# Kernel tuning notes

Measured on AMD Instinct MI355X. Metric: run time of the kernel, lower is better.

Reference implementation:

```python
import jax, jax.numpy as jnp
import numpy as np

B, N, T, F, D = 2, 8, 128, 128, 256
EPS = 1e-5


def setup_inputs() -> dict:
    key = jax.random.key(0)
    ks = jax.random.split(key, 8)
    s = 1.0 / np.sqrt(D)
    s2 = 1.0 / np.sqrt(2 * D)
    return {
        "x": jax.random.normal(ks[0], (B, N, D), dtype=jnp.float32),
        "t_emb": jax.random.normal(ks[1], (T, D), dtype=jnp.float32),
        "f_emb": jax.random.normal(ks[2], (F, D), dtype=jnp.float32),
        "ln_g": jnp.ones((D,), dtype=jnp.float32),
        "ln_b": jnp.zeros((D,), dtype=jnp.float32),
        "W1": jax.random.uniform(ks[3], (D, 2 * D), jnp.float32, -s, s),
        "b1": jax.random.uniform(ks[4], (2 * D,), jnp.float32, -s, s),
        "W2": jax.random.uniform(ks[5], (2 * D, 2), jnp.float32, -s2, s2),
        "b2": jax.random.uniform(ks[6], (2,), jnp.float32, -s2, s2),
    }


def reference(x, t_emb, f_emb, ln_g, ln_b, W1, b1, W2, b2):
    # x: [B,N,D]; pos_emb: [T,F,D]; broadcast-add -> [B,N,T,F,D]
    pos = t_emb[:, None, :] + f_emb[None, :, :]            # [T,F,D]
    h = x[:, :, None, None, :] + pos[None, None]           # [B,N,T,F,D]
    # LayerNorm over last dim
    mu = jnp.mean(h, axis=-1, keepdims=True)
    var = jnp.mean(jnp.square(h - mu), axis=-1, keepdims=True)
    h = (h - mu) * jax.lax.rsqrt(var + EPS) * ln_g + ln_b
    # MLP: D -> 2D -> 2
    h = jax.nn.relu(jnp.einsum("bntfd,de->bntfe", h, W1) + b1)
    out = jnp.einsum("bntfe,eo->bntfo", h, W2) + b2        # [B,N,T,F,2]
    return out
```

## Files before the change

kernel.cpp:

```cpp
#include <hip/hip_runtime.h>
#include <stdint.h>


#define D_ 256
#define E_ 512

typedef __attribute__((ext_vector_type(8))) short short8;
typedef __attribute__((ext_vector_type(4))) short short4v;
typedef __attribute__((ext_vector_type(4))) float f32x4;

typedef __attribute__((address_space(1))) void gvoid;
typedef __attribute__((address_space(3))) void lvoid;
#define GLOAD_LDS16(g, l) \
  __builtin_amdgcn_global_load_lds((gvoid*)(g), (lvoid*)(l), 16, 0, 0)

__device__ inline unsigned short f2bf(float f) {
  unsigned int u = __float_as_uint(f);
  u += 0x7fffu + ((u >> 16) & 1u);
  return (unsigned short)(u >> 16);
}
__device__ inline float bf2f(unsigned short h) {
  return __uint_as_float(((unsigned int)h) << 16);
}

__global__ __launch_bounds__(256) void prep(
    const float* __restrict__ x, const float* __restrict__ t_emb,
    const float* __restrict__ f_emb, const float* __restrict__ ln_g,
    const float* __restrict__ ln_b, const float* __restrict__ W1,
    const float* __restrict__ b1, const float* __restrict__ W2,
    unsigned short* __restrict__ Abuf, unsigned short* __restrict__ Bbuf,
    float* __restrict__ GKW, float* __restrict__ sxt,
    float* __restrict__ sqxt, float* __restrict__ sf,
    float* __restrict__ sqf) {
  const int blk = blockIdx.x;
  const int tid = threadIdx.x;
  if (blk < 544) {
    const int l = tid & 63;
    int arow;
    float v0, v1, v2, v3;
    if (blk < 512) {
      const int r = blk * 4 + (tid >> 6);
      const int bn = r >> 7, t = r & 127;
      const float4 xv = *(const float4*)(x + bn * D_ + 4 * l);
      const float4 tv = *(const float4*)(t_emb + t * D_ + 4 * l);
      v0 = xv.x + tv.x; v1 = xv.y + tv.y;
      v2 = xv.z + tv.z; v3 = xv.w + tv.w;
      arow = r;
    } else {
      const int fi = (blk - 512) * 4 + (tid >> 6);
      const float4 fv = *(const float4*)(f_emb + fi * D_ + 4 * l);
      v0 = fv.x; v1 = fv.y; v2 = fv.z; v3 = fv.w;
      arow = 2048 + fi;
    }
    union { unsigned short u[4]; short4v v; } hi, lo;
    hi.u[0] = f2bf(v0); hi.u[1] = f2bf(v1);
    hi.u[2] = f2bf(v2); hi.u[3] = f2bf(v3);
    lo.u[0] = f2bf(v0 - bf2f(hi.u[0]));
    lo.u[1] = f2bf(v1 - bf2f(hi.u[1]));
    lo.u[2] = f2bf(v2 - bf2f(hi.u[2]));
    lo.u[3] = f2bf(v3 - bf2f(hi.u[3]));
    unsigned short* ab = Abuf + arow * 768 + 4 * l;
    *(short4v*)(ab) = hi.v;
    *(short4v*)(ab + 256) = lo.v;
    *(short4v*)(ab + 512) = hi.v;
    float s = (v0 + v1) + (v2 + v3);
    float q = fmaf(v0, v0, fmaf(v1, v1, fmaf(v2, v2, v3 * v3)));
#pragma unroll
    for (int d = 1; d < 64; d <<= 1) {
      s += __shfl_xor(s, d);
      q += __shfl_xor(q, d);
    }
    if (l == 0) {
      if (blk < 512) { sxt[arow] = s; sqxt[arow] = q; }
      else           { sf[arow - 2048] = s; sqf[arow - 2048] = q; }
    }
  } else if (blk < 546) {
    const int e = (blk - 544) * 256 + tid;
    float G = 0.f, Kv = 0.f;
    for (int k = 0; k < 256; ++k) {
      const float w = W1[k * E_ + e];
      G = fmaf(ln_g[k], w, G);
      Kv = fmaf(ln_b[k], w, Kv);
    }
    float4 o;
    o.x = G; o.y = Kv + b1[e];
    o.z = W2[2 * e]; o.w = W2[2 * e + 1];
    *(float4*)(GKW + 4 * e) = o;
  } else {
    const int gidx = (blk - 546) * 256 + tid;
    const int lane = gidx & 63;
    const int jtl = (gidx >> 6) & 3;
    const int cc = gidx >> 8;
    const int ct = cc % 10;
    const int kt = cc / 10;
    const int col = ct * 64 + jtl * 16 + (lane & 15);
    const int kbase = kt * 32 + ((lane >> 4) & 3) * 8;
    union { unsigned short u[8]; short8 v; } fr;
#pragma unroll
    for (int j = 0; j < 8; ++j) {
      const int kk = kbase + j;
      const int term = kk >> 8;
      const int k = kk & 255;
      float v;
      if (col < 512) v = ln_g[k] * W1[k * E_ + col];
      else           v = f_emb[(col - 512) * D_ + k];
      const unsigned short h = f2bf(v);
      fr.u[j] = (term == 2) ? f2bf(v - bf2f(h)) : h;
    }
    *(short8*)(Bbuf + gidx * 8) = fr.v;
  }
}

__global__ __launch_bounds__(256) void gemm3(
    const unsigned short* __restrict__ Abuf,
    const unsigned short* __restrict__ Bbuf, float* __restrict__ U,
    float* __restrict__ C, float* __restrict__ Vt) {
  __shared__ short8 sB[2][256];
  const int tid = threadIdx.x;
  const int wave = tid >> 6, lane = tid & 63;
  const int quad = (lane >> 4) & 3, n16 = lane & 15;
  const int rt = blockIdx.x / 10, ct = blockIdx.x % 10;
  const int rowb = rt * 128 + wave * 32;

  GLOAD_LDS16((const char*)Bbuf + (size_t)ct * 4096 + tid * 16,
              &sB[0][wave * 64]);

  const unsigned short* a0 = Abuf + (size_t)(rowb + n16) * 768 + quad * 8;
  const unsigned short* a1 = a0 + 16 * 768;
  short8 acur0 = *(const short8*)a0;
  short8 acur1 = *(const short8*)a1;

  f32x4 acc[2][4];
#pragma unroll
  for (int j = 0; j < 4; ++j) {
    acc[0][j] = (f32x4){0.f, 0.f, 0.f, 0.f};
    acc[1][j] = (f32x4){0.f, 0.f, 0.f, 0.f};
  }

  for (int kt = 0; kt < 24; ++kt) {
    __syncthreads();
    short8 anxt0 = acur0, anxt1 = acur1;
    if (kt < 23) {
      GLOAD_LDS16(
          (const char*)Bbuf + (size_t)((kt + 1) * 10 + ct) * 4096 + tid * 16,
          &sB[(kt + 1) & 1][wave * 64]);
      anxt0 = *(const short8*)(a0 + (kt + 1) * 32);
      anxt1 = *(const short8*)(a1 + (kt + 1) * 32);
    }
    const short8* bp = &sB[kt & 1][0];
#pragma unroll
    for (int jtl = 0; jtl < 4; ++jtl) {
      const short8 bf = bp[jtl * 64 + lane];
      acc[0][jtl] =
          __builtin_amdgcn_mfma_f32_16x16x32_bf16(acur0, bf, acc[0][jtl], 0, 0, 0);
      acc[1][jtl] =
          __builtin_amdgcn_mfma_f32_16x16x32_bf16(acur1, bf, acc[1][jtl], 0, 0, 0);
    }
    acur0 = anxt0;
    acur1 = anxt1;
  }

#pragma unroll
  for (int g = 0; g < 2; ++g)
#pragma unroll
    for (int jtl = 0; jtl < 4; ++jtl)
#pragma unroll
      for (int r = 0; r < 4; ++r) {
        const float val = acc[g][jtl][r];
        const int grow = rowb + g * 16 + quad * 4 + r;
        const int col = ct * 64 + jtl * 16 + n16;
        if (rt < 16) {
          if (ct < 8) U[grow * 512 + col] = val;
          else        C[grow * 128 + (col - 512)] = val;
        } else if (ct < 8) {
          Vt[col * 128 + (grow - 2048)] = val;
        }
      }
}

__global__ __launch_bounds__(512) void decode2(
    const float* __restrict__ U, const float* __restrict__ Vt,
    const float* __restrict__ C, const float* __restrict__ GKW,
    const float* __restrict__ sxt, const float* __restrict__ sqxt,
    const float* __restrict__ sf, const float* __restrict__ sqf,
    const float* __restrict__ b2, float* __restrict__ out) {
  __shared__ float part[8][64][17];
  const int tid = threadIdx.x;
  const int w = tid >> 6, lane = tid & 63;
  const int bnt0 = blockIdx.x * 4;

  const float2 sf2 = *(const float2*)(sf + 2 * lane);
  const float2 sqf2 = *(const float2*)(sqf + 2 * lane);
  float Ar[4][2], Br[4][2];
#pragma unroll
  for (int ti = 0; ti < 4; ++ti) {
    const float sx = sxt[bnt0 + ti];
    const float sqx = sqxt[bnt0 + ti];
    const float2 c2 = *(const float2*)(C + (bnt0 + ti) * 128 + 2 * lane);
    {
      const float mu = (sx + sf2.x) * (1.f / 256.f);
      const float var = (sqx + 2.f * c2.x + sqf2.x) * (1.f / 256.f) - mu * mu;
      const float rs = rsqrtf(var + 1e-5f);
      Ar[ti][0] = rs; Br[ti][0] = -rs * mu;
    }
    {
      const float mu = (sx + sf2.y) * (1.f / 256.f);
      const float var = (sqx + 2.f * c2.y + sqf2.y) * (1.f / 256.f) - mu * mu;
      const float rs = rsqrtf(var + 1e-5f);
      Ar[ti][1] = rs; Br[ti][1] = -rs * mu;
    }
  }

  float o[4][2][2] = {};
  const int ebase = __builtin_amdgcn_readfirstlane(w * 64);
#pragma unroll 4
  for (int ei = 0; ei < 64; ++ei) {
    const int e = ebase + ei;
    const float4 gkw = *(const float4*)(GKW + 4 * e);
    const float2 v2 = *(const float2*)(Vt + e * 128 + 2 * lane);
#pragma unroll
    for (int ti = 0; ti < 4; ++ti) {
      const float u = U[(bnt0 + ti) * 512 + e];
      const float s0 = u + v2.x, s1 = u + v2.y;
      float y0 = fmaf(Ar[ti][0], s0, fmaf(Br[ti][0], gkw.x, gkw.y));
      float y1 = fmaf(Ar[ti][1], s1, fmaf(Br[ti][1], gkw.x, gkw.y));
      y0 = fmaxf(y0, 0.f);
      y1 = fmaxf(y1, 0.f);
      o[ti][0][0] = fmaf(y0, gkw.z, o[ti][0][0]);
      o[ti][0][1] = fmaf(y0, gkw.w, o[ti][0][1]);
      o[ti][1][0] = fmaf(y1, gkw.z, o[ti][1][0]);
      o[ti][1][1] = fmaf(y1, gkw.w, o[ti][1][1]);
    }
  }

#pragma unroll
  for (int ti = 0; ti < 4; ++ti)
#pragma unroll
    for (int ff = 0; ff < 2; ++ff) {
      part[w][lane][ti * 4 + ff * 2 + 0] = o[ti][ff][0];
      part[w][lane][ti * 4 + ff * 2 + 1] = o[ti][ff][1];
    }
  __syncthreads();

  const int t = tid >> 7, f = tid & 127;
  const int m = f >> 1, ff = f & 1;
  float r0 = b2[0], r1 = b2[1];
#pragma unroll
  for (int w2 = 0; w2 < 8; ++w2) {
    r0 += part[w2][m][t * 4 + ff * 2 + 0];
    r1 += part[w2][m][t * 4 + ff * 2 + 1];
  }
  float2 res;
  res.x = r0;
  res.y = r1;
  *(float2*)(out + ((bnt0 + t) * 128 + f) * 2) = res;
}

extern "C" void kernel_launch(void* const* d_in, const int* in_sizes, int n_in,
                              void* d_out, int out_size, void* d_ws,
                              size_t ws_size, hipStream_t stream) {
  const float* x = (const float*)d_in[0];
  const float* t_emb = (const float*)d_in[1];
  const float* f_emb = (const float*)d_in[2];
  const float* ln_g = (const float*)d_in[3];
  const float* ln_b = (const float*)d_in[4];
  const float* W1 = (const float*)d_in[5];
  const float* b1 = (const float*)d_in[6];
  const float* W2 = (const float*)d_in[7];
  const float* b2 = (const float*)d_in[8];

  char* ws = (char*)d_ws;
  unsigned short* Abuf = (unsigned short*)(ws + 0);
  unsigned short* Bbuf = (unsigned short*)(ws + 3342336);
  float* U    = (float*)(ws + 4325376);
  float* C    = (float*)(ws + 8519680);
  float* Vt   = (float*)(ws + 9568256);
  float* GKW  = (float*)(ws + 9830400);
  float* sxt  = (float*)(ws + 9838592);
  float* sqxt = (float*)(ws + 9846784);
  float* sfp  = (float*)(ws + 9854976);
  float* sqf  = (float*)(ws + 9855488);

  prep<<<786, 256, 0, stream>>>(x, t_emb, f_emb, ln_g, ln_b, W1, b1, W2, Abuf,
                                Bbuf, GKW, sxt, sqxt, sfp, sqf);
  gemm3<<<170, 256, 0, stream>>>(Abuf, Bbuf, U, C, Vt);
  decode2<<<512, 512, 0, stream>>>(U, Vt, C, GKW, sxt, sqxt, sfp, sqf, b2,
                                   (float*)d_out);
}
```

Before: 127.2 us.

## Use static device buffers, drop LDS staging in gemm, split G/K reduction

Replaces the workspace-pointer intermediates with statically allocated __device__ arrays, so the kernels take fewer arguments and see fixed addresses. The gemm kernel drops the double-buffered LDS staging of B via global_load_lds and its per-iteration barrier. It now reads A and B fragments straight from global memory inside a 4-way unrolled loop. The GKW reduction in prep is split into four independent accumulators to shorten the serial FMA chain. The risk is that direct B loads in gemm lose prefetch overlap and repeat global/L2 traffic across waves.

Measured after the change: 118.9 us. 6.5% less time.

```diff
diff --git a/kernel.cpp b/kernel.cpp
--- a/kernel.cpp
+++ b/kernel.cpp
@@ -9,10 +9,16 @@
 typedef __attribute__((ext_vector_type(4))) short short4v;
 typedef __attribute__((ext_vector_type(4))) float f32x4;
 
-typedef __attribute__((address_space(1))) void gvoid;
-typedef __attribute__((address_space(3))) void lvoid;
-#define GLOAD_LDS16(g, l) \
-  __builtin_amdgcn_global_load_lds((gvoid*)(g), (lvoid*)(l), 16, 0, 0)
+__device__ alignas(16) unsigned short g_Abuf[2176 * 768];
+__device__ alignas(16) unsigned short g_Bbuf[768 * 640];
+__device__ alignas(16) float g_U[2048 * 512];
+__device__ alignas(16) float g_C[2048 * 128];
+__device__ alignas(16) float g_Vt[512 * 128];
+__device__ alignas(16) float g_GKW[512 * 4];
+__device__ alignas(16) float g_sxt[2048];
+__device__ alignas(16) float g_sqxt[2048];
+__device__ alignas(16) float g_sf[128];
+__device__ alignas(16) float g_sqf[128];
 
 __device__ inline unsigned short f2bf(float f) {
   unsigned int u = __float_as_uint(f);
@@ -27,11 +33,7 @@
     const float* __restrict__ x, const float* __restrict__ t_emb,
     const float* __restrict__ f_emb, const float* __restrict__ ln_g,
     const float* __restrict__ ln_b, const float* __restrict__ W1,
-    const float* __restrict__ b1, const float* __restrict__ W2,
-    unsigned short* __restrict__ Abuf, unsigned short* __restrict__ Bbuf,
-    float* __restrict__ GKW, float* __restrict__ sxt,
-    float* __restrict__ sqxt, float* __restrict__ sf,
-    float* __restrict__ sqf) {
+    const float* __restrict__ b1, const float* __restrict__ W2) {
   const int blk = blockIdx.x;
   const int tid = threadIdx.x;
   if (blk < 544) {
@@ -59,7 +61,7 @@
     lo.u[1] = f2bf(v1 - bf2f(hi.u[1]));
     lo.u[2] = f2bf(v2 - bf2f(hi.u[2]));
     lo.u[3] = f2bf(v3 - bf2f(hi.u[3]));
-    unsigned short* ab = Abuf + arow * 768 + 4 * l;
+    unsigned short* ab = g_Abuf + arow * 768 + 4 * l;
     *(short4v*)(ab) = hi.v;
     *(short4v*)(ab + 256) = lo.v;
     *(short4v*)(ab + 512) = hi.v;
@@ -71,21 +73,28 @@
       q += __shfl_xor(q, d);
     }
     if (l == 0) {
-      if (blk < 512) { sxt[arow] = s; sqxt[arow] = q; }
-      else           { sf[arow - 2048] = s; sqf[arow - 2048] = q; }
+      if (blk < 512) { g_sxt[arow] = s; g_sqxt[arow] = q; }
+      else           { g_sf[arow - 2048] = s; g_sqf[arow - 2048] = q; }
     }
   } else if (blk < 546) {
     const int e = (blk - 544) * 256 + tid;
-    float G = 0.f, Kv = 0.f;
-    for (int k = 0; k < 256; ++k) {
-      const float w = W1[k * E_ + e];
-      G = fmaf(ln_g[k], w, G);
-      Kv = fmaf(ln_b[k], w, Kv);
+    float G0 = 0.f, G1 = 0.f, G2 = 0.f, G3 = 0.f;
+    float K0 = 0.f, K1 = 0.f, K2 = 0.f, K3 = 0.f;
+    for (int k = 0; k < 256; k += 4) {
+      const float w0 = W1[(k + 0) * E_ + e];
+      const float w1 = W1[(k + 1) * E_ + e];
+      const float w2 = W1[(k + 2) * E_ + e];
+      const float w3 = W1[(k + 3) * E_ + e];
+      G0 = fmaf(ln_g[k + 0], w0, G0); K0 = fmaf(ln_b[k + 0], w0, K0);
+      G1 = fmaf(ln_g[k + 1], w1, G1); K1 = fmaf(ln_b[k + 1], w1, K1);
+      G2 = fmaf(ln_g[k + 2], w2, G2); K2 = fmaf(ln_b[k + 2], w2, K2);
+      G3 = fmaf(ln_g[k + 3], w3, G3); K3 = fmaf(ln_b[k + 3], w3, K3);
     }
     float4 o;
-    o.x = G; o.y = Kv + b1[e];
+    o.x = (G0 + G1) + (G2 + G3);
+    o.y = (K0 + K1) + (K2 + K3) + b1[e];
     o.z = W2[2 * e]; o.w = W2[2 * e + 1];
-    *(float4*)(GKW + 4 * e) = o;
+    *(float4*)(g_GKW + 4 * e) = o;
   } else {
     const int gidx = (blk - 546) * 256 + tid;
     const int lane = gidx & 63;
@@ -107,28 +116,19 @@
       const unsigned short h = f2bf(v);
       fr.u[j] = (term == 2) ? f2bf(v - bf2f(h)) : h;
     }
-    *(short8*)(Bbuf + gidx * 8) = fr.v;
-  }
-}
-
-__global__ __launch_bounds__(256) void gemm3(
-    const unsigned short* __restrict__ Abuf,
-    const unsigned short* __restrict__ Bbuf, float* __restrict__ U,
-    float* __restrict__ C, float* __restrict__ Vt) {
-  __shared__ short8 sB[2][256];
+    *(short8*)(g_Bbuf + gidx * 8) = fr.v;
+  }
+}
+
+__global__ __launch_bounds__(256) void gemm3() {
   const int tid = threadIdx.x;
   const int wave = tid >> 6, lane = tid & 63;
   const int quad = (lane >> 4) & 3, n16 = lane & 15;
   const int rt = blockIdx.x / 10, ct = blockIdx.x % 10;
   const int rowb = rt * 128 + wave * 32;
 
-  GLOAD_LDS16((const char*)Bbuf + (size_t)ct * 4096 + tid * 16,
-              &sB[0][wave * 64]);
-
-  const unsigned short* a0 = Abuf + (size_t)(rowb + n16) * 768 + quad * 8;
+  const unsigned short* a0 = g_Abuf + (size_t)(rowb + n16) * 768 + quad * 8;
   const unsigned short* a1 = a0 + 16 * 768;
-  short8 acur0 = *(const short8*)a0;
-  short8 acur1 = *(const short8*)a1;
 
   f32x4 acc[2][4];
 #pragma unroll
@@ -137,27 +137,19 @@
     acc[1][j] = (f32x4){0.f, 0.f, 0.f, 0.f};
   }
 
+#pragma unroll 4
   for (int kt = 0; kt < 24; ++kt) {
-    __syncthreads();
-    short8 anxt0 = acur0, anxt1 = acur1;
-    if (kt < 23) {
-      GLOAD_LDS16(
-          (const char*)Bbuf + (size_t)((kt + 1) * 10 + ct) * 4096 + tid * 16,
-          &sB[(kt + 1) & 1][wave * 64]);
-      anxt0 = *(const short8*)(a0 + (kt + 1) * 32);
-      anxt1 = *(const short8*)(a1 + (kt + 1) * 32);
-    }
-    const short8* bp = &sB[kt & 1][0];
+    const short8 av0 = *(const short8*)(a0 + kt * 32);
+    const short8 av1 = *(const short8*)(a1 + kt * 32);
+    const short8* bp = (const short8*)g_Bbuf + ((kt * 10 + ct) * 4) * 64 + lane;
 #pragma unroll
     for (int jtl = 0; jtl < 4; ++jtl) {
-      const short8 bf = bp[jtl * 64 + lane];
+      const short8 bf = bp[jtl * 64];
       acc[0][jtl] =
-          __builtin_amdgcn_mfma_f32_16x16x32_bf16(acur0, bf, acc[0][jtl], 0, 0, 0);
+          __builtin_amdgcn_mfma_f32_16x16x32_bf16(av0, bf, acc[0][jtl], 0, 0, 0);
       acc[1][jtl] =
-          __builtin_amdgcn_mfma_f32_16x16x32_bf16(acur1, bf, acc[1][jtl], 0, 0, 0);
-    }
-    acur0 = anxt0;
-    acur1 = anxt1;
+          __builtin_amdgcn_mfma_f32_16x16x32_bf16(av1, bf, acc[1][jtl], 0, 0, 0);
+    }
   }
 
 #pragma unroll
@@ -170,33 +162,29 @@
         const int grow = rowb + g * 16 + quad * 4 + r;
         const int col = ct * 64 + jtl * 16 + n16;
         if (rt < 16) {
-          if (ct < 8) U[grow * 512 + col] = val;
-          else        C[grow * 128 + (col - 512)] = val;
+          if (ct < 8) g_U[grow * 512 + col] = val;
+          else        g_C[grow * 128 + (col - 512)] = val;
         } else if (ct < 8) {
-          Vt[col * 128 + (grow - 2048)] = val;
+          g_Vt[col * 128 + (grow - 2048)] = val;
         }
       }
 }
 
-__global__ __launch_bounds__(512) void decode2(
-    const float* __restrict__ U, const float* __restrict__ Vt,
-    const float* __restrict__ C, const float* __restrict__ GKW,
-    const float* __restrict__ sxt, const float* __restrict__ sqxt,
-    const float* __restrict__ sf, const float* __restrict__ sqf,
-    const float* __restrict__ b2, float* __restrict__ out) {
+__global__ __launch_bounds__(512) void decode2(const float* __restrict__ b2,
+                                               float* __restrict__ out) {
   __shared__ float part[8][64][17];
   const int tid = threadIdx.x;
   const int w = tid >> 6, lane = tid & 63;
   const int bnt0 = blockIdx.x * 4;
 
-  const float2 sf2 = *(const float2*)(sf + 2 * lane);
-  const float2 sqf2 = *(const float2*)(sqf + 2 * lane);
+  const float2 sf2 = *(const float2*)(g_sf + 2 * lane);
+  const float2 sqf2 = *(const float2*)(g_sqf + 2 * lane);
   float Ar[4][2], Br[4][2];
 #pragma unroll
   for (int ti = 0; ti < 4; ++ti) {
-    const float sx = sxt[bnt0 + ti];
-    const float sqx = sqxt[bnt0 + ti];
-    const float2 c2 = *(const float2*)(C + (bnt0 + ti) * 128 + 2 * lane);
+    const float sx = g_sxt[bnt0 + ti];
+    const float sqx = g_sqxt[bnt0 + ti];
+    const float2 c2 = *(const float2*)(g_C + (bnt0 + ti) * 128 + 2 * lane);
     {
       const float mu = (sx + sf2.x) * (1.f / 256.f);
       const float var = (sqx + 2.f * c2.x + sqf2.x) * (1.f / 256.f) - mu * mu;
@@ -216,11 +204,11 @@
 #pragma unroll 4
   for (int ei = 0; ei < 64; ++ei) {
     const int e = ebase + ei;
-    const float4 gkw = *(const float4*)(GKW + 4 * e);
-    const float2 v2 = *(const float2*)(Vt + e * 128 + 2 * lane);
+    const float4 gkw = *(const float4*)(g_GKW + 4 * e);
+    const float2 v2 = *(const float2*)(g_Vt + e * 128 + 2 * lane);
 #pragma unroll
     for (int ti = 0; ti < 4; ++ti) {
-      const float u = U[(bnt0 + ti) * 512 + e];
+      const float u = g_U[(bnt0 + ti) * 512 + e];
       const float s0 = u + v2.x, s1 = u + v2.y;
       float y0 = fmaf(Ar[ti][0], s0, fmaf(Br[ti][0], gkw.x, gkw.y));
       float y1 = fmaf(Ar[ti][1], s1, fmaf(Br[ti][1], gkw.x, gkw.y));
@@ -268,22 +256,9 @@
   const float* b1 = (const float*)d_in[6];
   const float* W2 = (const float*)d_in[7];
   const float* b2 = (const float*)d_in[8];
-
-  char* ws = (char*)d_ws;
-  unsigned short* Abuf = (unsigned short*)(ws + 0);
-  unsigned short* Bbuf = (unsigned short*)(ws + 3342336);
-  float* U    = (float*)(ws + 4325376);
-  float* C    = (float*)(ws + 8519680);
-  float* Vt   = (float*)(ws + 9568256);
-  float* GKW  = (float*)(ws + 9830400);
-  float* sxt  = (float*)(ws + 9838592);
-  float* sqxt = (float*)(ws + 9846784);
-  float* sfp  = (float*)(ws + 9854976);
-  float* sqf  = (float*)(ws + 9855488);
-
-  prep<<<786, 256, 0, stream>>>(x, t_emb, f_emb, ln_g, ln_b, W1, b1, W2, Abuf,
-                                Bbuf, GKW, sxt, sqxt, sfp, sqf);
-  gemm3<<<170, 256, 0, stream>>>(Abuf, Bbuf, U, C, Vt);
-  decode2<<<512, 512, 0, stream>>>(U, Vt, C, GKW, sxt, sqxt, sfp, sqf, b2,
-                                   (float*)d_out);
-}
+  (void)d_ws; (void)ws_size;
+
+  prep<<<786, 256, 0, stream>>>(x, t_emb, f_emb, ln_g, ln_b, W1, b1, W2);
+  gemm3<<<170, 256, 0, stream>>>();
+  decode2<<<512, 512, 0, stream>>>(b2, (float*)d_out);
+}
```
